# Kernel tuning notes

Hardware: AMD Instinct MI355X
Metric: run time of the kernel (lower is better)

Reference implementation:

```python
import jax, jax.numpy as jnp
import numpy as np


def setup_inputs() -> dict:
    key = jax.random.key(0)
    k1, k2, k3, k4, k5 = jax.random.split(key, 5)
    in_f, out_f, rank = 4096, 4096, 16
    std = 1.0 / np.sqrt(rank)
    x = jax.random.normal(k1, (4, 2048, in_f), dtype=jnp.float32)
    base_weight = jax.random.normal(k2, (out_f, in_f), dtype=jnp.float32) * 0.02
    lora_A = jax.random.normal(k3, (rank, in_f), dtype=jnp.float32) * std
    lora_B = jax.random.normal(k4, (out_f, rank), dtype=jnp.float32) * 0.01
    magnitude_vec = jax.random.uniform(k5, (out_f,), dtype=jnp.float32) + 0.5
    return {"x": x, "base_weight": base_weight, "lora_A": lora_A,
            "lora_B": lora_B, "magnitude_vec": magnitude_vec}


def reference(x, base_weight, lora_A, lora_B, magnitude_vec):
    # x: [B, S, in] -> tokens [N, in]
    out_shape = (*x.shape[:-1], base_weight.shape[0])
    xt = x.reshape(-1, x.shape[-1])
    # low-rank adapter path: [N, rank] @ [rank, out]
    lora_out = (xt @ lora_A.T) @ lora_B.T
    # column-wise L2 norm of adapted weight, per output row: [out]
    adapted_w = base_weight + lora_B @ lora_A
    column_norm = jnp.linalg.norm(adapted_w, axis=1)
    magnitude_scale = magnitude_vec / column_norm  # [out]
    # base GEMM + adapter + magnitude rescale epilogue
    dora_out = (xt @ base_weight.T + lora_out) * magnitude_scale[None, :]
    return dora_out.reshape(out_shape)
```

## Files before the change

kernel.cpp:

```cpp
#include <hip/hip_runtime.h>
#include <hip/hip_bf16.h>
#include <stdint.h>

typedef __attribute__((ext_vector_type(8))) short s16x8;
typedef __attribute__((ext_vector_type(4))) float f32x4;
typedef __attribute__((ext_vector_type(4))) unsigned short us4;

__device__ inline unsigned short bf_rne(float f) {
    union { float f; uint32_t u; } v; v.f = f;
    uint32_t u = v.u;
    u += 0x7FFFu + ((u >> 16) & 1u);
    return (unsigned short)(u >> 16);
}

#define GLD_LDS16(gp, lp)                                                     \
    __builtin_amdgcn_global_load_lds(                                         \
        (const __attribute__((address_space(1))) void*)(gp),                  \
        (__attribute__((address_space(3))) void*)(lp), 16, 0, 0)

#define LDSOFF(p) ((unsigned)(uintptr_t)(__attribute__((address_space(3))) const void*)(p))

__global__ __launch_bounds__(256) void prologue_kernel(
    const float4* __restrict__ x4, us4* __restrict__ xbf4,
    const float4* __restrict__ W4,
    const float4* __restrict__ A4,
    const float* __restrict__ B,
    const float* __restrict__ mag,
    unsigned short* __restrict__ wbf,
    float* __restrict__ scale) {
    const int tid = threadIdx.x;
    if (blockIdx.x < 512) {
        const int m0 = blockIdx.x * 8;
        __shared__ float Bs[8][16];
        __shared__ float red[32];
        if (tid < 128) Bs[tid >> 4][tid & 15] = B[m0 * 16 + tid];
        __syncthreads();
        float ss[8] = {};
        for (int c = tid; c < 1024; c += 256) {
            float4 a[16];
#pragma unroll
            for (int r = 0; r < 16; ++r) a[r] = A4[r * 1024 + c];
#pragma unroll
            for (int i = 0; i < 8; ++i) {
                float4 w = W4[(size_t)(m0 + i) * 1024 + c];
#pragma unroll
                for (int r = 0; r < 16; ++r) {
                    const float br = Bs[i][r];
                    w.x += br * a[r].x; w.y += br * a[r].y;
                    w.z += br * a[r].z; w.w += br * a[r].w;
                }
                ss[i] += w.x * w.x + w.y * w.y + w.z * w.z + w.w * w.w;
                us4 o; o[0] = bf_rne(w.x); o[1] = bf_rne(w.y);
                o[2] = bf_rne(w.z); o[3] = bf_rne(w.w);
                *(us4*)&wbf[(size_t)(m0 + i) * 4096 + c * 4] = o;
            }
        }
        const int lane = tid & 63, wv = tid >> 6;
#pragma unroll
        for (int i = 0; i < 8; ++i) {
            float v = ss[i];
#pragma unroll
            for (int off = 32; off > 0; off >>= 1) v += __shfl_down(v, off, 64);
            if (lane == 0) red[wv * 8 + i] = v;
        }
        __syncthreads();
        if (tid < 8) {
            float tot = red[tid] + red[8 + tid] + red[16 + tid] + red[24 + tid];
            scale[m0 + tid] = mag[m0 + tid] / sqrtf(tot);
        }
    } else {
        const size_t base = (size_t)(blockIdx.x - 512) * 1024 + tid;
#pragma unroll
        for (int j = 0; j < 4; ++j) {
            const size_t idx = base + j * 256;
            float4 a = x4[idx];
            us4 o;
            o[0] = bf_rne(a.x); o[1] = bf_rne(a.y);
            o[2] = bf_rne(a.z); o[3] = bf_rne(a.w);
            xbf4[idx] = o;
        }
    }
}

#define FENCE() asm volatile("" ::: "memory")
#define BAR()   do { FENCE(); __builtin_amdgcn_s_barrier(); FENCE(); } while (0)
#define VMW6()  asm volatile("s_waitcnt vmcnt(6)" ::: "memory")
#define VMW0()  asm volatile("s_waitcnt vmcnt(0)" ::: "memory")
#define LGW8()  asm volatile("s_waitcnt lgkmcnt(8)" ::: "memory")
#define LGW0()  asm volatile("s_waitcnt lgkmcnt(0)" ::: "memory")
#define SB0()   __builtin_amdgcn_sched_barrier(0)
#define PRIO1() __builtin_amdgcn_s_setprio(1)
#define PRIO0() __builtin_amdgcn_s_setprio(0)

#define DSR(dst, va, IMM) \
    asm volatile("ds_read_b128 %0, %1 offset:" #IMM : "=v"(dst) : "v"(va))

__global__ __launch_bounds__(512, 2) void dora_gemm(
    const unsigned short* __restrict__ xbf,
    const unsigned short* __restrict__ wbf,
    const float* __restrict__ scale,
    float* __restrict__ out) {
    __shared__ __align__(16) unsigned short As[2][256 * 64];
    __shared__ __align__(16) unsigned short Bs[2][256 * 64];

    const int tid  = threadIdx.x;
    const int lane = tid & 63;
    const int w    = tid >> 6;
    const int wm   = w >> 2;
    const int wn   = w & 3;
    const int q    = lane >> 4;
    const int c15  = lane & 15;

    const int bid = blockIdx.x;
    const int xcd = bid & 7, sub = bid >> 3;
    const int tileM = (((xcd & 3) << 3) | (sub & 7)) << 8;
    const int tileN = (((xcd >> 2) << 3) | (sub >> 3)) << 8;

    const int r0 = tid >> 3;
    const int lc = (tid & 7) ^ (r0 & 7);
    const size_t aoff = (size_t)(tileM + r0) * 4096 + lc * 8;
    const size_t boff = (size_t)(tileN + r0) * 4096 + lc * 8;
    const int ld0 = (w * 64) * 8;
    const int ld1 = (512 + w * 64) * 8;

#define STAGE_A(d, h, k0) do {                                                            \
    GLD_LDS16(xbf + aoff + (size_t)((h) * 128) * 4096 + (k0),      &As[d][(h) * 8192 + ld0]); \
    GLD_LDS16(xbf + aoff + (size_t)((h) * 128 + 64) * 4096 + (k0), &As[d][(h) * 8192 + ld1]); \
} while (0)
#define STAGE_B(d, h, k0) do {                                                            \
    GLD_LDS16(wbf + boff + (size_t)((h) * 128) * 4096 + (k0),      &Bs[d][(h) * 8192 + ld0]); \
    GLD_LDS16(wbf + boff + (size_t)((h) * 128 + 64) * 4096 + (k0), &Bs[d][(h) * 8192 + ld1]); \
} while (0)

    const int rb = c15 & 7;
    unsigned aA[4][2], aB[2][2];
#pragma unroll
    for (int mt = 0; mt < 4; ++mt)
#pragma unroll
        for (int kc = 0; kc < 2; ++kc)
            aA[mt][kc] = LDSOFF(&As[0][(wm * 64 + mt * 16 + c15) * 64 +
                                       ((kc * 4 + q) ^ rb) * 8]);
#pragma unroll
    for (int nt = 0; nt < 2; ++nt)
#pragma unroll
        for (int kc = 0; kc < 2; ++kc)
            aB[nt][kc] = LDSOFF(&Bs[0][(wn * 32 + nt * 16 + c15) * 64 +
                                       ((kc * 4 + q) ^ rb) * 8]);

    s16x8 af[4][2];
    s16x8 bfx[2][2][2];
    f32x4 acc[8][4] = {};

#define RD_A(IMM) do {                                                        \
    DSR(af[0][0], aA[0][0], IMM); DSR(af[0][1], aA[0][1], IMM);               \
    DSR(af[1][0], aA[1][0], IMM); DSR(af[1][1], aA[1][1], IMM);               \
    DSR(af[2][0], aA[2][0], IMM); DSR(af[2][1], aA[2][1], IMM);               \
    DSR(af[3][0], aA[3][0], IMM); DSR(af[3][1], aA[3][1], IMM); } while (0)
#define RD_B(nh, IMM) do {                                                    \
    DSR(bfx[nh][0][0], aB[0][0], IMM); DSR(bfx[nh][0][1], aB[0][1], IMM);     \
    DSR(bfx[nh][1][0], aB[1][0], IMM); DSR(bfx[nh][1][1], aB[1][1], IMM); } while (0)

#define MFMA_Q(mh, nh) do {                                                   \
    _Pragma("unroll") for (int mt = 0; mt < 4; ++mt)                          \
    _Pragma("unroll") for (int nt = 0; nt < 2; ++nt)                          \
    _Pragma("unroll") for (int kc = 0; kc < 2; ++kc)                          \
        acc[(mh) * 4 + mt][(nh) * 2 + nt] =                                   \
            __builtin_amdgcn_mfma_f32_16x16x32_bf16(                          \
                af[mt][kc], bfx[nh][nt][kc],                                  \
                acc[(mh) * 4 + mt][(nh) * 2 + nt], 0, 0, 0);                  \
} while (0)

    STAGE_A(0, 0, 0); STAGE_B(0, 0, 0); STAGE_B(0, 1, 0); STAGE_A(0, 1, 0);
    STAGE_A(1, 0, 64); STAGE_B(1, 0, 64); STAGE_B(1, 1, 64);
    VMW6(); BAR();

    for (int t0k = 0; t0k < 62 * 64; t0k += 128) {
        const int kA1 = t0k + 64;
        const int kn2 = t0k + 128;
        const int kn3 = t0k + 192;
        RD_A(0); RD_B(0, 0);
        STAGE_A(1, 1, kA1);
        LGW8(); BAR(); LGW0(); SB0();
        PRIO1(); MFMA_Q(0, 0); PRIO0(); BAR();
        RD_B(1, 16384);
        STAGE_A(0, 0, kn2);
        BAR(); LGW0(); SB0();
        PRIO1(); MFMA_Q(0, 1); PRIO0(); BAR();
        RD_A(16384);
        STAGE_B(0, 0, kn2);
        BAR(); LGW0(); SB0();
        PRIO1(); MFMA_Q(1, 1); PRIO0(); BAR();
        STAGE_B(0, 1, kn2);
        VMW6(); BAR();
        PRIO1(); MFMA_Q(1, 0); PRIO0(); BAR();
        RD_A(32768); RD_B(0, 32768);
        STAGE_A(0, 1, kn2);
        LGW8(); BAR(); LGW0(); SB0();
        PRIO1(); MFMA_Q(0, 0); PRIO0(); BAR();
        RD_B(1, 49152);
        STAGE_A(1, 0, kn3);
        BAR(); LGW0(); SB0();
        PRIO1(); MFMA_Q(0, 1); PRIO0(); BAR();
        RD_A(49152);
        STAGE_B(1, 0, kn3);
        BAR(); LGW0(); SB0();
        PRIO1(); MFMA_Q(1, 1); PRIO0(); BAR();
        STAGE_B(1, 1, kn3);
        VMW6(); BAR();
        PRIO1(); MFMA_Q(1, 0); PRIO0(); BAR();
    }

    RD_A(0); RD_B(0, 0);
    STAGE_A(1, 1, 63 * 64);
    LGW8(); BAR(); LGW0(); SB0();
    PRIO1(); MFMA_Q(0, 0); PRIO0(); BAR();
    RD_B(1, 16384);
    BAR(); LGW0(); SB0();
    PRIO1(); MFMA_Q(0, 1); PRIO0(); BAR();
    RD_A(16384);
    BAR(); LGW0(); SB0();
    PRIO1(); MFMA_Q(1, 1); PRIO0(); BAR();
    VMW0(); BAR();
    PRIO1(); MFMA_Q(1, 0); PRIO0(); BAR();
    RD_A(32768); RD_B(0, 32768);
    BAR(); LGW0(); SB0();
    PRIO1(); MFMA_Q(0, 0); PRIO0(); BAR();
    RD_B(1, 49152);
    BAR(); LGW0(); SB0();
    PRIO1(); MFMA_Q(0, 1); PRIO0(); BAR();
    RD_A(49152);
    LGW0(); SB0();
    PRIO1(); MFMA_Q(1, 1); PRIO0();
    MFMA_Q(1, 0);

#pragma unroll
    for (int nh = 0; nh < 2; ++nh)
#pragma unroll
    for (int nt = 0; nt < 2; ++nt) {
        const int col = tileN + nh * 128 + wn * 32 + nt * 16 + c15;
        const float s = scale[col];
#pragma unroll
        for (int mh = 0; mh < 2; ++mh)
#pragma unroll
        for (int mt = 0; mt < 4; ++mt) {
            const int row0 = tileM + mh * 128 + wm * 64 + mt * 16 + q * 4;
#pragma unroll
            for (int r = 0; r < 4; ++r)
                out[(size_t)(row0 + r) * 4096 + col] = acc[mh * 4 + mt][nh * 2 + nt][r] * s;
        }
    }
}

extern "C" void kernel_launch(void* const* d_in, const int* in_sizes, int n_in,
                              void* d_out, int out_size, void* d_ws, size_t ws_size,
                              hipStream_t stream) {
    const float* x   = (const float*)d_in[0];
    const float* W   = (const float*)d_in[1];
    const float* A   = (const float*)d_in[2];
    const float* B   = (const float*)d_in[3];
    const float* mag = (const float*)d_in[4];
    float* out = (float*)d_out;

    const size_t XBF_BYTES = (size_t)8192 * 4096 * 2;
    const size_t WBF_BYTES = (size_t)4096 * 4096 * 2;
    const size_t NEEDED = XBF_BYTES + WBF_BYTES + 4096 * sizeof(float);
    if (ws_size < NEEDED) return;

    unsigned short* xbf = (unsigned short*)d_ws;
    unsigned short* wbf = (unsigned short*)((char*)d_ws + XBF_BYTES);
    float* scale = (float*)((char*)d_ws + XBF_BYTES + WBF_BYTES);

    prologue_kernel<<<8704, 256, 0, stream>>>((const float4*)x, (us4*)xbf,
                                              (const float4*)W, (const float4*)A,
                                              B, mag, wbf, scale);
    dora_gemm<<<512, 512, 0, stream>>>(xbf, wbf, scale, out);
}
```

Baseline: 313.2 us.

## Reorder GEMM stage schedule and drop per-quadrant trailing barriers

Restructures the 8-phase double-buffered main loop so the second half of each k-tile is staged one phase later and loads are spread more evenly. It removes the trailing barrier after each MFMA quadrant, leaving one barrier per phase, and relaxes the vmcnt wait from 6 to 4. The intent is to cut synchronisation overhead and keep LDS reads, global-to-LDS loads and MFMA overlapping. With fewer barriers there is a risk of LDS write/read races if any buffer reuse ordering is now only implicitly protected.

```diff
diff --git a/kernel.cpp b/kernel.cpp
--- a/kernel.cpp
+++ b/kernel.cpp
@@ -84,9 +84,8 @@
 
 #define FENCE() asm volatile("" ::: "memory")
 #define BAR()   do { FENCE(); __builtin_amdgcn_s_barrier(); FENCE(); } while (0)
-#define VMW6()  asm volatile("s_waitcnt vmcnt(6)" ::: "memory")
+#define VMW4()  asm volatile("s_waitcnt vmcnt(4)" ::: "memory")
 #define VMW0()  asm volatile("s_waitcnt vmcnt(0)" ::: "memory")
-#define LGW8()  asm volatile("s_waitcnt lgkmcnt(8)" ::: "memory")
 #define LGW0()  asm volatile("s_waitcnt lgkmcnt(0)" ::: "memory")
 #define SB0()   __builtin_amdgcn_sched_barrier(0)
 #define PRIO1() __builtin_amdgcn_s_setprio(1)
@@ -171,67 +170,66 @@
 } while (0)
 
     STAGE_A(0, 0, 0); STAGE_B(0, 0, 0); STAGE_B(0, 1, 0); STAGE_A(0, 1, 0);
-    STAGE_A(1, 0, 64); STAGE_B(1, 0, 64); STAGE_B(1, 1, 64);
-    VMW6(); BAR();
-
-    for (int t0k = 0; t0k < 62 * 64; t0k += 128) {
-        const int kA1 = t0k + 64;
+    STAGE_A(1, 0, 64); STAGE_B(1, 0, 64);
+    VMW4(); BAR();
+
+    for (int t0k = 0; t0k <= 60 * 64; t0k += 128) {
+        const int kt1 = t0k + 64;
         const int kn2 = t0k + 128;
         const int kn3 = t0k + 192;
         RD_A(0); RD_B(0, 0);
-        STAGE_A(1, 1, kA1);
-        LGW8(); BAR(); LGW0(); SB0();
-        PRIO1(); MFMA_Q(0, 0); PRIO0(); BAR();
+        STAGE_B(1, 1, kt1);
+        BAR(); LGW0(); SB0();
+        PRIO1(); MFMA_Q(0, 0); PRIO0();
         RD_B(1, 16384);
+        STAGE_A(1, 1, kt1);
+        BAR(); LGW0(); SB0();
+        PRIO1(); MFMA_Q(0, 1); PRIO0();
+        RD_A(16384);
         STAGE_A(0, 0, kn2);
         BAR(); LGW0(); SB0();
-        PRIO1(); MFMA_Q(0, 1); PRIO0(); BAR();
-        RD_A(16384);
+        PRIO1(); MFMA_Q(1, 1); PRIO0();
         STAGE_B(0, 0, kn2);
-        BAR(); LGW0(); SB0();
-        PRIO1(); MFMA_Q(1, 1); PRIO0(); BAR();
+        VMW4(); BAR();
+        PRIO1(); MFMA_Q(1, 0); PRIO0();
+        RD_A(32768); RD_B(0, 32768);
         STAGE_B(0, 1, kn2);
-        VMW6(); BAR();
-        PRIO1(); MFMA_Q(1, 0); PRIO0(); BAR();
-        RD_A(32768); RD_B(0, 32768);
+        BAR(); LGW0(); SB0();
+        PRIO1(); MFMA_Q(0, 0); PRIO0();
+        RD_B(1, 49152);
         STAGE_A(0, 1, kn2);
-        LGW8(); BAR(); LGW0(); SB0();
-        PRIO1(); MFMA_Q(0, 0); PRIO0(); BAR();
-        RD_B(1, 49152);
+        BAR(); LGW0(); SB0();
+        PRIO1(); MFMA_Q(0, 1); PRIO0();
+        RD_A(49152);
         STAGE_A(1, 0, kn3);
         BAR(); LGW0(); SB0();
-        PRIO1(); MFMA_Q(0, 1); PRIO0(); BAR();
-        RD_A(49152);
+        PRIO1(); MFMA_Q(1, 1); PRIO0();
         STAGE_B(1, 0, kn3);
-        BAR(); LGW0(); SB0();
-        PRIO1(); MFMA_Q(1, 1); PRIO0(); BAR();
-        STAGE_B(1, 1, kn3);
-        VMW6(); BAR();
-        PRIO1(); MFMA_Q(1, 0); PRIO0(); BAR();
+        VMW4(); BAR();
+        PRIO1(); MFMA_Q(1, 0); PRIO0();
     }
 
     RD_A(0); RD_B(0, 0);
-    STAGE_A(1, 1, 63 * 64);
-    LGW8(); BAR(); LGW0(); SB0();
-    PRIO1(); MFMA_Q(0, 0); PRIO0(); BAR();
+    STAGE_B(1, 1, 4032);
+    LGW0(); SB0();
+    PRIO1(); MFMA_Q(0, 0); PRIO0();
     RD_B(1, 16384);
-    BAR(); LGW0(); SB0();
-    PRIO1(); MFMA_Q(0, 1); PRIO0(); BAR();
+    STAGE_A(1, 1, 4032);
+    LGW0(); SB0();
+    PRIO1(); MFMA_Q(0, 1); PRIO0();
     RD_A(16384);
-    BAR(); LGW0(); SB0();
-    PRIO1(); MFMA_Q(1, 1); PRIO0(); BAR();
+    LGW0(); SB0();
+    PRIO1(); MFMA_Q(1, 1); MFMA_Q(1, 0); PRIO0();
     VMW0(); BAR();
-    PRIO1(); MFMA_Q(1, 0); PRIO0(); BAR();
     RD_A(32768); RD_B(0, 32768);
-    BAR(); LGW0(); SB0();
-    PRIO1(); MFMA_Q(0, 0); PRIO0(); BAR();
+    LGW0(); SB0();
+    PRIO1(); MFMA_Q(0, 0); PRIO0();
     RD_B(1, 49152);
-    BAR(); LGW0(); SB0();
-    PRIO1(); MFMA_Q(0, 1); PRIO0(); BAR();
+    LGW0(); SB0();
+    PRIO1(); MFMA_Q(0, 1); PRIO0();
     RD_A(49152);
     LGW0(); SB0();
-    PRIO1(); MFMA_Q(1, 1); PRIO0();
-    MFMA_Q(1, 0);
+    PRIO1(); MFMA_Q(1, 1); MFMA_Q(1, 0); PRIO0();
 
 #pragma unroll
     for (int nh = 0; nh < 2; ++nh)
```

Measured after the change: 303.6 us. 3.1% less time.
